# Optimization experiments

Measured on AMD Instinct MI355X. Metric: run time of the kernel, lower is better.

## Reference

```python
import jax, jax.numpy as jnp
from jax import lax
import numpy as np

NPOINT, RADIUS, NSAMPLE = 1024, 0.2, 32
MLP, IN_CH, EPS = (64, 64, 128), 6, 1e-5
B, N = 8, 4096


def farthest_point_sample(xyz, npoint):
    # xyz: [B, N, 3] -> idx [B, npoint]. Deterministic start at index 0.
    Bn, Nn, _ = xyz.shape
    def body(carry, _):
        dist, farthest = carry  # dist [B,N], farthest [B]
        centroid = jnp.take_along_axis(xyz, farthest[:, None, None], axis=1)  # [B,1,3]
        d = jnp.sum((xyz - centroid) ** 2, axis=-1)  # [B,N]
        dist = jnp.minimum(dist, d)
        return (dist, jnp.argmax(dist, axis=-1).astype(jnp.int32)), farthest
    init = (jnp.full((Bn, Nn), 1e10, xyz.dtype), jnp.zeros((Bn,), jnp.int32))
    _, idx = lax.scan(body, init, None, length=npoint)  # [npoint, B]
    return idx.T


def query_ball_point(radius, nsample, xyz, new_xyz):
    # xyz [B,N,3], new_xyz [B,S,3] -> idx [B,S,nsample]
    Bn, Nn, _ = xyz.shape
    sq = (jnp.sum(new_xyz ** 2, -1)[:, :, None]
          + jnp.sum(xyz ** 2, -1)[:, None, :]
          - 2.0 * jnp.einsum('bsc,bnc->bsn', new_xyz, xyz))  # [B,S,N]
    gidx = jnp.where(sq > radius ** 2, Nn, jnp.arange(Nn, dtype=jnp.int32)[None, None, :])
    gidx = jnp.sort(gidx, axis=-1)[:, :, :nsample]
    first = gidx[:, :, :1]
    return jnp.where(gidx == Nn, first, gidx)


def setup_inputs():
    key = jax.random.key(0)
    ks = jax.random.split(key, 8)
    inp = {
        'xyz': jax.random.uniform(ks[0], (B, 3, N), dtype=jnp.float32),
        'points': jax.random.normal(ks[1], (B, 3, N), dtype=jnp.float32),
    }
    last = IN_CH
    for i, oc in enumerate(MLP):
        inp[f'w{i}'] = jax.random.normal(ks[2 + i], (oc, last), dtype=jnp.float32) * 0.1
        inp[f'b{i}'] = jnp.zeros((oc,), jnp.float32)
        inp[f'g{i}'] = jnp.ones((oc,), jnp.float32)
        inp[f'be{i}'] = jnp.zeros((oc,), jnp.float32)
        last = oc
    return inp


def reference(xyz, points, w0, b0, g0, be0, w1, b1, g1, be1, w2, b2, g2, be2):
    x = jnp.transpose(xyz, (0, 2, 1))      # [B,N,3]
    p = jnp.transpose(points, (0, 2, 1))   # [B,N,D]
    fidx = farthest_point_sample(x, NPOINT)                       # [B,S]
    new_xyz = jnp.take_along_axis(x, fidx[:, :, None], axis=1)    # [B,S,3]
    idx = query_ball_point(RADIUS, NSAMPLE, x, new_xyz)           # [B,S,K]
    gather = jax.vmap(lambda a, i: a[i])                          # per-batch gather
    grouped_xyz = gather(x, idx)                                  # [B,S,K,3]
    grouped_xyz_norm = grouped_xyz - new_xyz[:, :, None, :]
    grouped_points = gather(p, idx)                               # [B,S,K,D]
    feat = jnp.concatenate([grouped_xyz_norm, grouped_points], axis=-1)  # [B,S,K,C]
    for w, b, g, be in ((w0, b0, g0, be0), (w1, b1, g1, be1), (w2, b2, g2, be2)):
        feat = jnp.einsum('bskc,oc->bsko', feat, w) + b
        mean = feat.mean(axis=(0, 1, 2))
        var = feat.var(axis=(0, 1, 2))
        feat = (feat - mean) * lax.rsqrt(var + EPS) * g + be  # BatchNorm (training stats)
        feat = jax.nn.relu(feat)
    new_points = jnp.max(feat, axis=2)                            # max over K -> [B,S,Cout]
    return jnp.transpose(new_xyz, (0, 2, 1)), jnp.transpose(new_points, (0, 2, 1))
```

## Files before the change

kernel.cpp:

```cpp
#include <hip/hip_runtime.h>
#include <stdint.h>

#define NPTS   4096
#define NPOINT 1024
#define NSAMP  32
#define NROWS  262144
#define RAD2   0.04f

typedef float v2f __attribute__((ext_vector_type(2)));
typedef __attribute__((ext_vector_type(8))) short bf16x8;
typedef __attribute__((ext_vector_type(4))) float f32x4;

__device__ __forceinline__ unsigned short f2bf(float x) {
    unsigned u = __float_as_uint(x);
    return (unsigned short)((u + 0x7FFFu + ((u >> 16) & 1u)) >> 16);
}
__device__ __forceinline__ unsigned pack2bf(float a, float b) {
    return (unsigned)f2bf(a) | ((unsigned)f2bf(b) << 16);
}

#define DPPMAX(v, C)                                                           \
    fmaxf(__int_as_float(__builtin_amdgcn_update_dpp(                          \
              0, __float_as_int(v), C, 0xf, 0xf, true)),                       \
          (v))

__global__ __launch_bounds__(256) void fps_kernel(const float* __restrict__ xyz,
                                                  float* __restrict__ outx)
{
    __shared__ __align__(16) float4 pxyz[NPTS];
    __shared__ __align__(16) float4 orec[NPOINT];
    __shared__ __align__(16) unsigned long long wkey[2][4];
    const int b = blockIdx.x, tid = threadIdx.x;
    const int lane = tid & 63, wid = tid >> 6;
    const float* base = xyz + b * 3 * NPTS;

    float Xs[16], Ys[16], Zs[16];
#pragma unroll
    for (int j = 0; j < 16; ++j) {
        const int n = j * 256 + tid;
        Xs[j] = base[n];
        Ys[j] = base[NPTS + n];
        Zs[j] = base[2 * NPTS + n];
        pxyz[n] = make_float4(Xs[j], Ys[j], Zs[j], 0.0f);
    }
    v2f X2[8], Y2[8], Z2[8], D2[8];
#pragma unroll
    for (int j = 0; j < 8; ++j) {
        X2[j] = (v2f){Xs[2 * j], Xs[2 * j + 1]};
        Y2[j] = (v2f){Ys[2 * j], Ys[2 * j + 1]};
        Z2[j] = (v2f){Zs[2 * j], Zs[2 * j + 1]};
        D2[j] = (v2f){1e10f, 1e10f};
    }
    __syncthreads();
    float4 c4 = pxyz[0];
    float cx = c4.x, cy = c4.y, cz = c4.z;

    for (int t = 0; t < NPOINT; ++t) {
        if (tid == 0) orec[t] = make_float4(cx, cy, cz, 0.0f);
        const v2f cxv = (v2f){cx, cx}, cyv = (v2f){cy, cy}, czv = (v2f){cz, cz};
        float bv = -1.0f; int bi = 0;
#pragma unroll
        for (int j = 0; j < 8; ++j) {
            v2f nd;
            {
#pragma clang fp contract(off)
                const v2f dx = X2[j] - cxv;
                const v2f dy = Y2[j] - cyv;
                const v2f dz = Z2[j] - czv;
                const v2f m0 = dx * dx;
                const v2f m1 = dy * dy;
                const v2f m2 = dz * dz;
                const v2f d = (m0 + m1) + m2;
                nd = __builtin_elementwise_min(D2[j], d);
            }
            D2[j] = nd;
            if (nd.x > bv) { bv = nd.x; bi = j * 512 + tid; }
            if (nd.y > bv) { bv = nd.y; bi = j * 512 + 256 + tid; }
        }
        float rv = bv;
        rv = DPPMAX(rv, 0x111);
        rv = DPPMAX(rv, 0x112);
        rv = DPPMAX(rv, 0x114);
        rv = DPPMAX(rv, 0x118);
        rv = DPPMAX(rv, 0x142);
        rv = DPPMAX(rv, 0x143);
        const unsigned wmax =
            (unsigned)__builtin_amdgcn_readlane(__float_as_int(rv), 63);
        unsigned long long mask = __ballot(__float_as_uint(bv) == wmax);
        unsigned best =
            (unsigned)__builtin_amdgcn_readlane(bi, (int)__builtin_ctzll(mask));
        mask &= mask - 1ull;
        while (mask) {
            const unsigned cand = (unsigned)__builtin_amdgcn_readlane(
                bi, (int)__builtin_ctzll(mask));
            best = cand < best ? cand : best;
            mask &= mask - 1ull;
        }
        if (lane == 0)
            wkey[t & 1][wid] = ((unsigned long long)wmax << 32) |
                               (unsigned)(~best);
        __syncthreads();
        const ulonglong2* wk = (const ulonglong2*)wkey[t & 1];
        const ulonglong2 ka = wk[0], kb = wk[1];
        unsigned long long kk = ka.x;
        if (ka.y > kk) kk = ka.y;
        if (kb.x > kk) kk = kb.x;
        if (kb.y > kk) kk = kb.y;
        const int farthest = (int)(~(unsigned)kk) & (NPTS - 1);
        c4 = pxyz[farthest];
        cx = c4.x; cy = c4.y; cz = c4.z;
    }
    __syncthreads();
    float* ox = outx + b * 3 * NPOINT;
    for (int i = tid; i < NPOINT; i += 256) {
        const float4 c = orec[i];
        ox[i]              = c.x;
        ox[NPOINT + i]     = c.y;
        ox[2 * NPOINT + i] = c.z;
    }
}

__global__ __launch_bounds__(256) void ball_kernel(const float* __restrict__ xyz,
                                                   const float* __restrict__ pts,
                                                   const float* __restrict__ outx,
                                                   int* __restrict__ idxbuf,
                                                   float* __restrict__ mom,
                                                   uint4* __restrict__ featbuf)
{
    __shared__ float red[4][42];
    const int tid = threadIdx.x;
    const int w = blockIdx.x * 4 + (tid >> 6);
    const int lane = tid & 63, wid = tid >> 6;
    const int b = w >> 10, s = w & 1023;
    const float* base = xyz + b * 3 * NPTS;
    const float cx = outx[b * 3 * NPOINT + s];
    const float cy = outx[b * 3 * NPOINT + NPOINT + s];
    const float cz = outx[b * 3 * NPOINT + 2 * NPOINT + s];
    const float sumS = __fadd_rn(__fadd_rn(__fmul_rn(cx, cx), __fmul_rn(cy, cy)),
                                 __fmul_rn(cz, cz));
    int cnt = 0, first_n = -1;
    int* myidx = idxbuf + w * NSAMP;

    for (int chunk = 0; chunk < NPTS / 64 && cnt < NSAMP; ++chunk) {
        const int n = chunk * 64 + lane;
        float nx = base[n], ny = base[NPTS + n], nz = base[2 * NPTS + n];
        float sumN = __fadd_rn(__fadd_rn(__fmul_rn(nx, nx), __fmul_rn(ny, ny)),
                               __fmul_rn(nz, nz));
        float dot = __fadd_rn(__fadd_rn(__fmul_rn(cx, nx), __fmul_rn(cy, ny)),
                              __fmul_rn(cz, nz));
        float sq = __fsub_rn(__fadd_rn(sumS, sumN), __fmul_rn(2.0f, dot));
        bool keep = (sq <= RAD2);
        unsigned long long mask = __ballot(keep);
        if (first_n < 0 && mask) first_n = chunk * 64 + (int)__builtin_ctzll(mask);
        int pos = cnt + __popcll(mask & ((1ull << lane) - 1ull));
        if (keep && pos < NSAMP) myidx[pos] = n;
        cnt += __popcll(mask);
    }
    if (cnt < NSAMP) {
        if (lane >= cnt && lane < NSAMP) myidx[lane] = first_n;
    }

    float m[42];
#pragma unroll
    for (int i = 0; i < 42; ++i) m[i] = 0.f;
    if (lane < 32) {
        const int idx = myidx[lane];
        const float* pb = pts + b * 3 * NPTS;
        float f[6];
        f[0] = base[idx] - cx;
        f[1] = base[NPTS + idx] - cy;
        f[2] = base[2 * NPTS + idx] - cz;
        f[3] = pb[idx];
        f[4] = pb[NPTS + idx];
        f[5] = pb[2 * NPTS + idx];
        featbuf[w * NSAMP + lane] =
            make_uint4(pack2bf(f[0], f[1]), pack2bf(f[2], f[3]),
                       pack2bf(f[4], f[5]), 0u);
#pragma unroll
        for (int c = 0; c < 6; ++c) m[c] = f[c];
#pragma unroll
        for (int c = 0; c < 6; ++c)
#pragma unroll
            for (int d = 0; d < 6; ++d)
                m[6 + c * 6 + d] = f[c] * f[d];
    }
#pragma unroll
    for (int i = 0; i < 42; ++i) {
        float v = m[i];
        v += __shfl_xor(v, 1);  v += __shfl_xor(v, 2);  v += __shfl_xor(v, 4);
        v += __shfl_xor(v, 8);  v += __shfl_xor(v, 16); v += __shfl_xor(v, 32);
        m[i] = v;
    }
    if (lane == 0) {
#pragma unroll
        for (int i = 0; i < 42; ++i) red[wid][i] = m[i];
    }
    __syncthreads();
    if (tid < 42)
        atomicAdd(&mom[tid], red[0][tid] + red[1][tid] + red[2][tid] + red[3][tid]);
}

__device__ __forceinline__ void compute_bn0(int o, const float* __restrict__ mom,
                                            const float* __restrict__ w0,
                                            const float* __restrict__ g,
                                            const float* __restrict__ be,
                                            float* __restrict__ sbn0)
{
    float w[6];
#pragma unroll
    for (int c = 0; c < 6; ++c) w[c] = w0[o * 6 + c];
    const float inv = 1.0f / (float)NROWS;
    float mean = 0.f;
#pragma unroll
    for (int c = 0; c < 6; ++c) mean = fmaf(w[c], mom[c], mean);
    mean *= inv;
    float ey2 = 0.f;
#pragma unroll
    for (int c = 0; c < 6; ++c) {
        float t = 0.f;
#pragma unroll
        for (int d = 0; d < 6; ++d) t = fmaf(w[d], mom[6 + c * 6 + d], t);
        ey2 = fmaf(w[c], t, ey2);
    }
    ey2 *= inv;
    const float var = ey2 - mean * mean;
    const float scale = g[o] * rsqrtf(var + 1e-5f);
    sbn0[o] = scale;
    sbn0[64 + o] = be[o] - mean * scale;
}

#define XP  72
#define WP  72
#define W0P 40

__global__ __launch_bounds__(256, 2) void mlp1_kernel(
    const uint4* __restrict__ featbuf,
    const float* __restrict__ w0, const float* __restrict__ mom,
    const float* __restrict__ g0, const float* __restrict__ be0,
    const float* __restrict__ w1, float* __restrict__ stats)
{
    __shared__ __align__(16) unsigned short sw0[64 * W0P];
    __shared__ __align__(16) unsigned short sw1[64 * WP];
    __shared__ __align__(16) unsigned short xb[4][32 * XP];
    __shared__ float sbn0[128];
    __shared__ float red[4][128];
    const int tid = threadIdx.x, lane = tid & 63, wid = tid >> 6;

    for (int i = tid; i < 64 * W0P / 2; i += 256) ((unsigned*)sw0)[i] = 0;
    if (tid < 64) compute_bn0(tid, mom, w0, g0, be0, sbn0);
    __syncthreads();
    for (int i = tid; i < 192; i += 256) {
        const int o = i / 3, c = (i % 3) * 2;
        *(unsigned*)&sw0[o * W0P + c] = pack2bf(w0[o * 6 + c], w0[o * 6 + c + 1]);
    }
    for (int i = tid; i < 2048; i += 256) {
        const int o = i >> 5, k = (i & 31) * 2;
        *(unsigned*)&sw1[o * WP + k] = pack2bf(w1[o * 64 + k], w1[o * 64 + k + 1]);
    }

    const int mh = lane & 15, q = lane >> 4;
    unsigned short* X = xb[wid];
    const int rbase = blockIdx.x * 512 + wid * 32;
    float sA[4] = {0.f, 0.f, 0.f, 0.f}, qA[4] = {0.f, 0.f, 0.f, 0.f};

    for (int c = 0; c < 4; ++c) {
        __syncthreads();
        if (lane < 32) {
            const int r = rbase + c * 128 + lane;
            uint4* xq = (uint4*)&xb[wid][lane * XP];
            xq[0] = featbuf[r];
            xq[1] = make_uint4(0u, 0u, 0u, 0u);
            xq[2] = make_uint4(0u, 0u, 0u, 0u);
            xq[3] = make_uint4(0u, 0u, 0u, 0u);
        }
        __syncthreads();
        f32x4 acc0[2][4] = {};
        {
            bf16x8 a[2], bw[4];
#pragma unroll
            for (int mt = 0; mt < 2; ++mt)
                a[mt] = *(const bf16x8*)&X[(mt * 16 + mh) * XP + q * 8];
#pragma unroll
            for (int nt = 0; nt < 4; ++nt)
                bw[nt] = *(const bf16x8*)&sw0[(nt * 16 + mh) * W0P + q * 8];
#pragma unroll
            for (int mt = 0; mt < 2; ++mt)
#pragma unroll
                for (int nt = 0; nt < 4; ++nt)
                    acc0[mt][nt] = __builtin_amdgcn_mfma_f32_16x16x32_bf16(
                        a[mt], bw[nt], acc0[mt][nt], 0, 0, 0);
        }
        __syncthreads();
#pragma unroll
        for (int nt = 0; nt < 4; ++nt) {
            const int ch = nt * 16 + mh;
            const float sc = sbn0[ch], sh = sbn0[64 + ch];
#pragma unroll
            for (int mt = 0; mt < 2; ++mt)
#pragma unroll
                for (int rr = 0; rr < 4; ++rr) {
                    const float v = fmaxf(fmaf(acc0[mt][nt][rr], sc, sh), 0.0f);
                    X[(mt * 16 + q * 4 + rr) * XP + ch] = f2bf(v);
                }
        }
        __syncthreads();
        f32x4 acc1[2][4] = {};
#pragma unroll
        for (int ks = 0; ks < 2; ++ks) {
            bf16x8 a[2], bw[4];
#pragma unroll
            for (int mt = 0; mt < 2; ++mt)
                a[mt] = *(const bf16x8*)&X[(mt * 16 + mh) * XP + ks * 32 + q * 8];
#pragma unroll
            for (int nt = 0; nt < 4; ++nt)
                bw[nt] = *(const bf16x8*)&sw1[(nt * 16 + mh) * WP + ks * 32 + q * 8];
#pragma unroll
            for (int mt = 0; mt < 2; ++mt)
#pragma unroll
                for (int nt = 0; nt < 4; ++nt)
                    acc1[mt][nt] = __builtin_amdgcn_mfma_f32_16x16x32_bf16(
                        a[mt], bw[nt], acc1[mt][nt], 0, 0, 0);
        }
#pragma unroll
        for (int nt = 0; nt < 4; ++nt)
#pragma unroll
            for (int mt = 0; mt < 2; ++mt)
#pragma unroll
                for (int rr = 0; rr < 4; ++rr) {
                    const float v = acc1[mt][nt][rr];
                    sA[nt] += v;
                    qA[nt] = fmaf(v, v, qA[nt]);
                }
    }
#pragma unroll
    for (int nt = 0; nt < 4; ++nt) {
        float s = sA[nt], qq = qA[nt];
        s += __shfl_xor(s, 16); qq += __shfl_xor(qq, 16);
        s += __shfl_xor(s, 32); qq += __shfl_xor(qq, 32);
        if (q == 0) {
            red[wid][nt * 16 + mh] = s;
            red[wid][64 + nt * 16 + mh] = qq;
        }
    }
    __syncthreads();
    if (tid < 128)
        atomicAdd(&stats[tid],
                  red[0][tid] + red[1][tid] + red[2][tid] + red[3][tid]);
}

__global__ __launch_bounds__(256, 2) void mlp2_kernel(
    const uint4* __restrict__ featbuf,
    const float* __restrict__ w0, const float* __restrict__ mom,
    const float* __restrict__ g0, const float* __restrict__ be0,
    const float* __restrict__ w1, const float* __restrict__ stats1,
    const float* __restrict__ g1, const float* __restrict__ be1,
    const float* __restrict__ w2,
    float* __restrict__ stats, float* __restrict__ gmax)
{
    __shared__ __align__(16) unsigned short sw0[64 * W0P];
    __shared__ __align__(16) unsigned short sw1[64 * WP];
    __shared__ __align__(16) unsigned short sw2[128 * WP];
    __shared__ __align__(16) unsigned short xb[4][32 * XP];
    __shared__ float sbn0[128];
    __shared__ float sbn1[128];
    __shared__ float red[4][256];
    const int tid = threadIdx.x, lane = tid & 63, wid = tid >> 6;

    for (int i = tid; i < 64 * W0P / 2; i += 256) ((unsigned*)sw0)[i] = 0;
    if (tid < 64) {
        compute_bn0(tid, mom, w0, g0, be0, sbn0);
    } else if (tid < 128) {
        const int ch = tid - 64;
        const float inv = 1.0f / (float)NROWS;
        const float mean = stats1[ch] * inv;
        const float var = stats1[64 + ch] * inv - mean * mean;
        const float scale = g1[ch] * rsqrtf(var + 1e-5f);
        sbn1[ch] = scale;
        sbn1[64 + ch] = be1[ch] - mean * scale;
    }
    __syncthreads();
    for (int i = tid; i < 192; i += 256) {
        const int o = i / 3, c = (i % 3) * 2;
        *(unsigned*)&sw0[o * W0P + c] = pack2bf(w0[o * 6 + c], w0[o * 6 + c + 1]);
    }
    for (int i = tid; i < 2048; i += 256) {
        const int o = i >> 5, k = (i & 31) * 2;
        *(unsigned*)&sw1[o * WP + k] = pack2bf(w1[o * 64 + k], w1[o * 64 + k + 1]);
    }
    for (int i = tid; i < 4096; i += 256) {
        const int o = i >> 5, k = (i & 31) * 2;
        *(unsigned*)&sw2[o * WP + k] = pack2bf(w2[o * 64 + k], w2[o * 64 + k + 1]);
    }

    const int mh = lane & 15, q = lane >> 4;
    unsigned short* X = xb[wid];
    const int rbase = blockIdx.x * 512 + wid * 32;
    float sA[8], qA[8];
#pragma unroll
    for (int i = 0; i < 8; ++i) { sA[i] = 0.f; qA[i] = 0.f; }

    for (int c = 0; c < 4; ++c) {
        __syncthreads();
        if (lane < 32) {
            const int r = rbase + c * 128 + lane;
            uint4* xq = (uint4*)&xb[wid][lane * XP];
            xq[0] = featbuf[r];
            xq[1] = make_uint4(0u, 0u, 0u, 0u);
            xq[2] = make_uint4(0u, 0u, 0u, 0u);
            xq[3] = make_uint4(0u, 0u, 0u, 0u);
        }
        __syncthreads();
        f32x4 acc0[2][4] = {};
        {
            bf16x8 a[2], bw[4];
#pragma unroll
            for (int mt = 0; mt < 2; ++mt)
                a[mt] = *(const bf16x8*)&X[(mt * 16 + mh) * XP + q * 8];
#pragma unroll
            for (int nt = 0; nt < 4; ++nt)
                bw[nt] = *(const bf16x8*)&sw0[(nt * 16 + mh) * W0P + q * 8];
#pragma unroll
            for (int mt = 0; mt < 2; ++mt)
#pragma unroll
                for (int nt = 0; nt < 4; ++nt)
                    acc0[mt][nt] = __builtin_amdgcn_mfma_f32_16x16x32_bf16(
                        a[mt], bw[nt], acc0[mt][nt], 0, 0, 0);
        }
        __syncthreads();
#pragma unroll
        for (int nt = 0; nt < 4; ++nt) {
            const int ch = nt * 16 + mh;
            const float sc = sbn0[ch], sh = sbn0[64 + ch];
#pragma unroll
            for (int mt = 0; mt < 2; ++mt)
#pragma unroll
                for (int rr = 0; rr < 4; ++rr) {
                    const float v = fmaxf(fmaf(acc0[mt][nt][rr], sc, sh), 0.0f);
                    X[(mt * 16 + q * 4 + rr) * XP + ch] = f2bf(v);
                }
        }
        __syncthreads();
        f32x4 acc1[2][4] = {};
#pragma unroll
        for (int ks = 0; ks < 2; ++ks) {
            bf16x8 a[2], bw[4];
#pragma unroll
            for (int mt = 0; mt < 2; ++mt)
                a[mt] = *(const bf16x8*)&X[(mt * 16 + mh) * XP + ks * 32 + q * 8];
#pragma unroll
            for (int nt = 0; nt < 4; ++nt)
                bw[nt] = *(const bf16x8*)&sw1[(nt * 16 + mh) * WP + ks * 32 + q * 8];
#pragma unroll
            for (int mt = 0; mt < 2; ++mt)
#pragma unroll
                for (int nt = 0; nt < 4; ++nt)
                    acc1[mt][nt] = __builtin_amdgcn_mfma_f32_16x16x32_bf16(
                        a[mt], bw[nt], acc1[mt][nt], 0, 0, 0);
        }
        __syncthreads();
#pragma unroll
        for (int nt = 0; nt < 4; ++nt) {
            const int ch = nt * 16 + mh;
            const float sc = sbn1[ch], sh = sbn1[64 + ch];
#pragma unroll
            for (int mt = 0; mt < 2; ++mt)
#pragma unroll
                for (int rr = 0; rr < 4; ++rr) {
                    const float v = fmaxf(fmaf(acc1[mt][nt][rr], sc, sh), 0.0f);
                    X[(mt * 16 + q * 4 + rr) * XP + ch] = f2bf(v);
                }
        }
        __syncthreads();
        const int g = blockIdx.x * 16 + c * 4 + wid;
        bf16x8 a2[2][2];
#pragma unroll
        for (int mt = 0; mt < 2; ++mt)
#pragma unroll
            for (int ks = 0; ks < 2; ++ks)
                a2[mt][ks] = *(const bf16x8*)&X[(mt * 16 + mh) * XP + ks * 32 + q * 8];
#pragma unroll
        for (int nt = 0; nt < 8; ++nt) {
            f32x4 acc[2] = {};
#pragma unroll
            for (int ks = 0; ks < 2; ++ks) {
                const bf16x8 bw = *(const bf16x8*)&sw2[(nt * 16 + mh) * WP + ks * 32 + q * 8];
#pragma unroll
                for (int mt = 0; mt < 2; ++mt)
                    acc[mt] = __builtin_amdgcn_mfma_f32_16x16x32_bf16(
                        a2[mt][ks], bw, acc[mt], 0, 0, 0);
            }
            float m = -3.0e38f;
#pragma unroll
            for (int mt = 0; mt < 2; ++mt)
#pragma unroll
                for (int rr = 0; rr < 4; ++rr) {
                    const float v = acc[mt][rr];
                    sA[nt] += v;
                    qA[nt] = fmaf(v, v, qA[nt]);
                    m = fmaxf(m, v);
                }
            m = fmaxf(m, __shfl_xor(m, 16));
            m = fmaxf(m, __shfl_xor(m, 32));
            if (q == 0) gmax[(nt * 16 + mh) * 8192 + g] = m;
        }
    }
#pragma unroll
    for (int nt = 0; nt < 8; ++nt) {
        float s = sA[nt], qq = qA[nt];
        s += __shfl_xor(s, 16); qq += __shfl_xor(qq, 16);
        s += __shfl_xor(s, 32); qq += __shfl_xor(qq, 32);
        if (q == 0) {
            red[wid][nt * 16 + mh] = s;
            red[wid][128 + nt * 16 + mh] = qq;
        }
    }
    __syncthreads();
    atomicAdd(&stats[tid],
              red[0][tid] + red[1][tid] + red[2][tid] + red[3][tid]);
}

__global__ __launch_bounds__(256) void final_kernel(const float* __restrict__ gmax,
                                                    const float* __restrict__ stats2,
                                                    const float* __restrict__ g2,
                                                    const float* __restrict__ be2,
                                                    float* __restrict__ out2)
{
    __shared__ float sbn[256];
    const int tid = threadIdx.x;
    if (tid < 128) {
        const float inv = 1.0f / (float)NROWS;
        const float mean = stats2[tid] * inv;
        const float var = stats2[128 + tid] * inv - mean * mean;
        const float scale = g2[tid] * rsqrtf(var + 1e-5f);
        sbn[tid] = scale;
        sbn[128 + tid] = be2[tid] - mean * scale;
    }
    __syncthreads();
    const int t = blockIdx.x * 256 + tid;
    const int s = t & 1023;
    const int o = (t >> 10) & 127;
    const int b = t >> 17;
    const int g = (b << 10) | s;
    float v = gmax[o * 8192 + g];
    v = fmaf(v, sbn[o], sbn[128 + o]);
    out2[t] = fmaxf(v, 0.0f);
}

extern "C" void kernel_launch(void* const* d_in, const int* in_sizes, int n_in,
                              void* d_out, int out_size, void* d_ws, size_t ws_size,
                              hipStream_t stream)
{
    const float* xyz = (const float*)d_in[0];
    const float* pts = (const float*)d_in[1];
    const float* w0  = (const float*)d_in[2];
    const float* g0  = (const float*)d_in[4];
    const float* be0 = (const float*)d_in[5];
    const float* w1  = (const float*)d_in[6];
    const float* g1  = (const float*)d_in[8];
    const float* be1 = (const float*)d_in[9];
    const float* w2  = (const float*)d_in[10];
    const float* g2  = (const float*)d_in[12];
    const float* be2 = (const float*)d_in[13];

    float* out_xyz = (float*)d_out;
    float* out2    = out_xyz + 8 * 3 * NPOINT;

    char* wsb = (char*)d_ws;
    int*   idxbuf  = (int*)(wsb + 32768);
    float* stats   = (float*)(wsb + 32768 + 1048576);
    float* gmax    = stats + 1024;
    uint4* featbuf = (uint4*)(gmax + 128 * 8192);

    float* mom    = stats;
    float* stats1 = stats + 128;
    float* stats2 = stats + 256;

    hipMemsetAsync(stats, 0, 512 * sizeof(float), stream);

    fps_kernel<<<8, 256, 0, stream>>>(xyz, out_xyz);
    ball_kernel<<<2048, 256, 0, stream>>>(xyz, pts, out_xyz, idxbuf, mom, featbuf);
    mlp1_kernel<<<512, 256, 0, stream>>>(featbuf, w0, mom, g0, be0, w1, stats1);
    mlp2_kernel<<<512, 256, 0, stream>>>(featbuf, w0, mom, g0, be0,
                                         w1, stats1, g1, be1,
                                         w2, stats2, gmax);
    final_kernel<<<4096, 256, 0, stream>>>(gmax, stats2, g2, be2, out2);
}
```

Measured before the change: 794.5 us.

## Run farthest-point sampling in a single wavefront per batch

The FPS kernel moves from four wavefronts per batch to one 64-lane wavefront holding all 4096 points in registers. This removes the per-iteration __syncthreads and the shared-memory cross-wave key reduction. The per-element argmax tracking is replaced by packed max reductions, and the index is recovered only on lanes that hold the maximum, by rescanning one quarter of the registers. In exchange each lane does four times more distance work per iteration on a single SIMD, and register pressure rises sharply.

```diff
diff --git a/kernel.cpp b/kernel.cpp
--- a/kernel.cpp
+++ b/kernel.cpp
@@ -24,59 +24,62 @@
               0, __float_as_int(v), C, 0xf, 0xf, true)),                       \
           (v))
 
-__global__ __launch_bounds__(256) void fps_kernel(const float* __restrict__ xyz,
-                                                  float* __restrict__ outx)
+__global__ __launch_bounds__(64) void fps_kernel(const float* __restrict__ xyz,
+                                                 float* __restrict__ outx)
 {
     __shared__ __align__(16) float4 pxyz[NPTS];
     __shared__ __align__(16) float4 orec[NPOINT];
-    __shared__ __align__(16) unsigned long long wkey[2][4];
-    const int b = blockIdx.x, tid = threadIdx.x;
-    const int lane = tid & 63, wid = tid >> 6;
+    const int b = blockIdx.x, lane = threadIdx.x;
     const float* base = xyz + b * 3 * NPTS;
 
-    float Xs[16], Ys[16], Zs[16];
-#pragma unroll
-    for (int j = 0; j < 16; ++j) {
-        const int n = j * 256 + tid;
-        Xs[j] = base[n];
-        Ys[j] = base[NPTS + n];
-        Zs[j] = base[2 * NPTS + n];
-        pxyz[n] = make_float4(Xs[j], Ys[j], Zs[j], 0.0f);
-    }
-    v2f X2[8], Y2[8], Z2[8], D2[8];
-#pragma unroll
-    for (int j = 0; j < 8; ++j) {
-        X2[j] = (v2f){Xs[2 * j], Xs[2 * j + 1]};
-        Y2[j] = (v2f){Ys[2 * j], Ys[2 * j + 1]};
-        Z2[j] = (v2f){Zs[2 * j], Zs[2 * j + 1]};
-        D2[j] = (v2f){1e10f, 1e10f};
-    }
-    __syncthreads();
+    v2f X2[32], Y2[32], Z2[32], D2[32];
+#pragma unroll
+    for (int p = 0; p < 32; ++p) {
+        const int n0 = p * 128 + lane;
+        const int n1 = n0 + 64;
+        const float x0 = base[n0], x1 = base[n1];
+        const float y0 = base[NPTS + n0], y1 = base[NPTS + n1];
+        const float z0 = base[2 * NPTS + n0], z1 = base[2 * NPTS + n1];
+        X2[p] = (v2f){x0, x1};
+        Y2[p] = (v2f){y0, y1};
+        Z2[p] = (v2f){z0, z1};
+        D2[p] = (v2f){1e10f, 1e10f};
+        pxyz[n0] = make_float4(x0, y0, z0, 0.0f);
+        pxyz[n1] = make_float4(x1, y1, z1, 0.0f);
+    }
     float4 c4 = pxyz[0];
     float cx = c4.x, cy = c4.y, cz = c4.z;
 
     for (int t = 0; t < NPOINT; ++t) {
-        if (tid == 0) orec[t] = make_float4(cx, cy, cz, 0.0f);
+        if (lane == 0) orec[t] = make_float4(cx, cy, cz, 0.0f);
         const v2f cxv = (v2f){cx, cx}, cyv = (v2f){cy, cy}, czv = (v2f){cz, cz};
-        float bv = -1.0f; int bi = 0;
-#pragma unroll
-        for (int j = 0; j < 8; ++j) {
+        v2f PM0 = (v2f){-1.f, -1.f}, PM1 = (v2f){-1.f, -1.f};
+        v2f PM2 = (v2f){-1.f, -1.f}, PM3 = (v2f){-1.f, -1.f};
+#pragma unroll
+        for (int p = 0; p < 32; ++p) {
             v2f nd;
             {
 #pragma clang fp contract(off)
-                const v2f dx = X2[j] - cxv;
-                const v2f dy = Y2[j] - cyv;
-                const v2f dz = Z2[j] - czv;
+                const v2f dx = X2[p] - cxv;
+                const v2f dy = Y2[p] - cyv;
+                const v2f dz = Z2[p] - czv;
                 const v2f m0 = dx * dx;
                 const v2f m1 = dy * dy;
                 const v2f m2 = dz * dz;
                 const v2f d = (m0 + m1) + m2;
-                nd = __builtin_elementwise_min(D2[j], d);
+                nd = __builtin_elementwise_min(D2[p], d);
             }
-            D2[j] = nd;
-            if (nd.x > bv) { bv = nd.x; bi = j * 512 + tid; }
-            if (nd.y > bv) { bv = nd.y; bi = j * 512 + 256 + tid; }
-        }
+            D2[p] = nd;
+            if (p < 8)       PM0 = __builtin_elementwise_max(PM0, nd);
+            else if (p < 16) PM1 = __builtin_elementwise_max(PM1, nd);
+            else if (p < 24) PM2 = __builtin_elementwise_max(PM2, nd);
+            else             PM3 = __builtin_elementwise_max(PM3, nd);
+        }
+        const float q0 = fmaxf(PM0.x, PM0.y);
+        const float q1 = fmaxf(PM1.x, PM1.y);
+        const float q2 = fmaxf(PM2.x, PM2.y);
+        const float q3 = fmaxf(PM3.x, PM3.y);
+        const float bv = fmaxf(fmaxf(q0, q1), fmaxf(q2, q3));
         float rv = bv;
         rv = DPPMAX(rv, 0x111);
         rv = DPPMAX(rv, 0x112);
@@ -87,8 +90,29 @@
         const unsigned wmax =
             (unsigned)__builtin_amdgcn_readlane(__float_as_int(rv), 63);
         unsigned long long mask = __ballot(__float_as_uint(bv) == wmax);
-        unsigned best =
-            (unsigned)__builtin_amdgcn_readlane(bi, (int)__builtin_ctzll(mask));
+        int bi = 0x7FFFFFFF;
+        if (__float_as_uint(bv) == wmax) {
+            const int qsel = (__float_as_uint(q0) == wmax) ? 0
+                           : (__float_as_uint(q1) == wmax) ? 1
+                           : (__float_as_uint(q2) == wmax) ? 2 : 3;
+            const int pbase = qsel * 8;
+#pragma unroll
+            for (int p = 0; p < 8; ++p) {
+                const v2f a0 = D2[p], a1 = D2[8 + p];
+                const v2f a2 = D2[16 + p], a3 = D2[24 + p];
+                const v2f dq = (qsel == 0) ? a0
+                             : (qsel == 1) ? a1
+                             : (qsel == 2) ? a2 : a3;
+                const int i0 = (pbase + p) * 128 + lane;
+                if (__float_as_uint(dq.x) == wmax) bi = (i0 < bi) ? i0 : bi;
+                if (__float_as_uint(dq.y) == wmax) {
+                    const int i1 = i0 + 64;
+                    bi = (i1 < bi) ? i1 : bi;
+                }
+            }
+        }
+        unsigned best = (unsigned)__builtin_amdgcn_readlane(
+            bi, (int)__builtin_ctzll(mask));
         mask &= mask - 1ull;
         while (mask) {
             const unsigned cand = (unsigned)__builtin_amdgcn_readlane(
@@ -96,23 +120,11 @@
             best = cand < best ? cand : best;
             mask &= mask - 1ull;
         }
-        if (lane == 0)
-            wkey[t & 1][wid] = ((unsigned long long)wmax << 32) |
-                               (unsigned)(~best);
-        __syncthreads();
-        const ulonglong2* wk = (const ulonglong2*)wkey[t & 1];
-        const ulonglong2 ka = wk[0], kb = wk[1];
-        unsigned long long kk = ka.x;
-        if (ka.y > kk) kk = ka.y;
-        if (kb.x > kk) kk = kb.x;
-        if (kb.y > kk) kk = kb.y;
-        const int farthest = (int)(~(unsigned)kk) & (NPTS - 1);
-        c4 = pxyz[farthest];
+        c4 = pxyz[best];
         cx = c4.x; cy = c4.y; cz = c4.z;
     }
-    __syncthreads();
     float* ox = outx + b * 3 * NPOINT;
-    for (int i = tid; i < NPOINT; i += 256) {
+    for (int i = lane; i < NPOINT; i += 64) {
         const float4 c = orec[i];
         ox[i]              = c.x;
         ox[NPOINT + i]     = c.y;
@@ -577,7 +589,7 @@
 
     hipMemsetAsync(stats, 0, 512 * sizeof(float), stream);
 
-    fps_kernel<<<8, 256, 0, stream>>>(xyz, out_xyz);
+    fps_kernel<<<8, 64, 0, stream>>>(xyz, out_xyz);
     ball_kernel<<<2048, 256, 0, stream>>>(xyz, pts, out_xyz, idxbuf, mom, featbuf);
     mlp1_kernel<<<512, 256, 0, stream>>>(featbuf, w0, mom, g0, be0, w1, stats1);
     mlp2_kernel<<<512, 256, 0, stream>>>(featbuf, w0, mom, g0, be0,
```

Result: slower. 1.740 ms (+119.0%).
